# Optimization experiments

Measured on AMD Instinct MI355X. Metric: run time of the kernel, lower is better.

## Reference

```python
import jax, jax.numpy as jnp
import numpy as np

D = 500  # hidden width hard-coded in the module

def _lrelu(x):
    # nn.LeakyReLU default negative_slope = 0.01
    return jnp.where(x > 0, x, 0.01 * x)

def setup_inputs() -> dict:
    key = jax.random.key(0)
    ks = jax.random.split(key, 20)
    T, B = 2048, 64
    inp = {
        "pitches": jax.random.normal(ks[0], (T, B, 128), dtype=jnp.float32),
        "velocities": jax.random.normal(ks[1], (T, B, 128), dtype=jnp.float32),
        "durations": jax.random.uniform(ks[2], (T, B, 1), dtype=jnp.float32),
        "steps": jax.random.uniform(ks[3], (T, B, 1), dtype=jnp.float32),
        # learned params (torch Linear convention: W is [out, in])
        "Wp": jax.random.normal(ks[4], (D, 128), dtype=jnp.float32) * 0.05,
        "bp": jax.random.normal(ks[5], (D,), dtype=jnp.float32) * 0.05,
        "Wv": jax.random.normal(ks[6], (D, 128), dtype=jnp.float32) * 0.05,
        "bv": jax.random.normal(ks[7], (D,), dtype=jnp.float32) * 0.05,
        "Wd": jax.random.normal(ks[8], (D, 1), dtype=jnp.float32) * 0.05,
        "bd": jax.random.normal(ks[9], (D,), dtype=jnp.float32) * 0.05,
        "Ws": jax.random.normal(ks[10], (D, 1), dtype=jnp.float32) * 0.05,
        "bs": jax.random.normal(ks[11], (D,), dtype=jnp.float32) * 0.05,
        "W1": jax.random.normal(ks[12], (D, D), dtype=jnp.float32) * 0.05,
        "b1": jax.random.normal(ks[13], (D,), dtype=jnp.float32) * 0.05,
        "W2": jax.random.normal(ks[14], (D, D), dtype=jnp.float32) * 0.05,
        "b2": jax.random.normal(ks[15], (D,), dtype=jnp.float32) * 0.05,
        "Wi": jax.random.normal(ks[16], (D, D), dtype=jnp.float32) * 0.05,
        "bi": jax.random.normal(ks[17], (D,), dtype=jnp.float32) * 0.05,
        "W3": jax.random.normal(ks[18], (1, D), dtype=jnp.float32) * 0.05,
        "b3": jax.random.normal(ks[19], (1,), dtype=jnp.float32) * 0.05,
    }
    return inp

def reference(pitches, velocities, durations, steps,
              Wp, bp, Wv, bv, Wd, bd, Ws, bs,
              W1, b1, W2, b2, Wi, bi, W3, b3):
    # Note: in the original torch code the LSTMCell output is computed then
    # discarded (overwritten), and `info` at step t depends only on inputs at
    # step t. Thus the final output depends only on the last timestep through
    # the embed-sum -> LeakyReLU MLP -> linear_intermediate chain.
    # Vectorized over all T timesteps (same per-step math as the loop body).
    add = (jnp.einsum('tbi,oi->tbo', pitches, Wp) + bp
           + jnp.einsum('tbi,oi->tbo', velocities, Wv) + bv
           + jnp.einsum('tbi,oi->tbo', durations, Wd) + bd
           + jnp.einsum('tbi,oi->tbo', steps, Ws) + bs)      # [T,B,500]
    h = _lrelu(jnp.einsum('tbi,oi->tbo', add, W1) + b1)
    h = _lrelu(jnp.einsum('tbi,oi->tbo', h, W2) + b2)
    info = jnp.einsum('tbi,oi->tbo', h, Wi) + bi              # [T,B,500]
    out = jax.nn.sigmoid(info[-1] @ W3.T + b3)                # [B,1]
    return out
```

## Files before the change

kernel.cpp:

```cpp
#include <hip/hip_runtime.h>

#define DD 500
#define BB 64
#define TT 2048
#define KP 128
#define VCHUNKS 32
#define VPSTRIDE 512

__global__ __launch_bounds__(256) void k_embed(
    const float* __restrict__ pitches, const float* __restrict__ velocities,
    const float* __restrict__ durations, const float* __restrict__ steps,
    const float* __restrict__ Wp, const float* __restrict__ bp,
    const float* __restrict__ Wv, const float* __restrict__ bv,
    const float* __restrict__ Wd, const float* __restrict__ bd,
    const float* __restrict__ Wst, const float* __restrict__ bs,
    float* __restrict__ addT)
{
    const int tid = threadIdx.x;
    const int bid = blockIdx.x;

    __shared__ float lds[KP * BB];
    const int b = tid & 63;
    const int o = __builtin_amdgcn_readfirstlane(bid * 4 + (tid >> 6));
    const float* __restrict__ wp = Wp + o * KP;
    const float* __restrict__ wv = Wv + o * KP;

    float a0 = 0.f, a1 = 0.f, a2 = 0.f, a3 = 0.f;

    const float4* Psrc = (const float4*)(pitches + (size_t)(TT - 1) * BB * KP);
    const float4* Vsrc = (const float4*)(velocities + (size_t)(TT - 1) * BB * KP);

    for (int j = tid; j < BB * KP / 4; j += 256) {
        float4 p = Psrc[j];
        int pb = j >> 5;
        int k0 = (j & 31) * 4;
        lds[(k0 + 0) * BB + ((pb + k0 + 0) & 63)] = p.x;
        lds[(k0 + 1) * BB + ((pb + k0 + 1) & 63)] = p.y;
        lds[(k0 + 2) * BB + ((pb + k0 + 2) & 63)] = p.z;
        lds[(k0 + 3) * BB + ((pb + k0 + 3) & 63)] = p.w;
    }
    __syncthreads();
    for (int k = 0; k < KP; k += 4) {
        a0 += lds[(k + 0) * BB + ((b + k + 0) & 63)] * wp[k + 0];
        a1 += lds[(k + 1) * BB + ((b + k + 1) & 63)] * wp[k + 1];
        a2 += lds[(k + 2) * BB + ((b + k + 2) & 63)] * wp[k + 2];
        a3 += lds[(k + 3) * BB + ((b + k + 3) & 63)] * wp[k + 3];
    }
    __syncthreads();

    for (int j = tid; j < BB * KP / 4; j += 256) {
        float4 p = Vsrc[j];
        int pb = j >> 5;
        int k0 = (j & 31) * 4;
        lds[(k0 + 0) * BB + ((pb + k0 + 0) & 63)] = p.x;
        lds[(k0 + 1) * BB + ((pb + k0 + 1) & 63)] = p.y;
        lds[(k0 + 2) * BB + ((pb + k0 + 2) & 63)] = p.z;
        lds[(k0 + 3) * BB + ((pb + k0 + 3) & 63)] = p.w;
    }
    __syncthreads();
    for (int k = 0; k < KP; k += 4) {
        a0 += lds[(k + 0) * BB + ((b + k + 0) & 63)] * wv[k + 0];
        a1 += lds[(k + 1) * BB + ((b + k + 1) & 63)] * wv[k + 1];
        a2 += lds[(k + 2) * BB + ((b + k + 2) & 63)] * wv[k + 2];
        a3 += lds[(k + 3) * BB + ((b + k + 3) & 63)] * wv[k + 3];
    }

    const float dur = durations[(size_t)(TT - 1) * BB + b];
    const float st  = steps[(size_t)(TT - 1) * BB + b];
    addT[o * BB + b] = bp[o] + bv[o] + bd[o] + bs[o]
                     + dur * Wd[o] + st * Wst[o]
                     + (a0 + a1) + (a2 + a3);
}

__global__ __launch_bounds__(256) void k_dense(
    const float* __restrict__ Ain, const float* __restrict__ W,
    const float* __restrict__ bias, float* __restrict__ Aout, int leaky,
    const float* __restrict__ Wi, const float* __restrict__ W3,
    float* __restrict__ vpart)
{
    const int tid = threadIdx.x;
    const int bid = blockIdx.x;

    if (bid >= DD) {
        const int oc = bid - DD;
        const int obeg = oc * 16;
        const int k0 = tid;
        const int k1 = tid + 256;
        float acc0 = 0.f, acc1 = 0.f;
        #pragma unroll
        for (int i = 0; i < 16; ++i) {
            const int o = obeg + i;
            const int oc_ = o < DD ? o : DD - 1;
            const float ww = o < DD ? W3[oc_] : 0.f;
            acc0 += ww * Wi[(size_t)oc_ * DD + k0];
            if (k1 < DD) acc1 += ww * Wi[(size_t)oc_ * DD + k1];
        }
        vpart[oc * VPSTRIDE + k0] = acc0;
        if (k1 < DD) vpart[oc * VPSTRIDE + k1] = acc1;
        return;
    }

    __shared__ float partial[4][BB];
    const int b = tid & 63;
    const int w = tid >> 6;
    const int o = bid;
    const float* __restrict__ wrow = W + o * DD;
    const int kbeg = w * 125;

    float a0 = 0.f, a1 = 0.f, a2 = 0.f, a3 = 0.f;
    float a4 = 0.f, a5 = 0.f, a6 = 0.f, a7 = 0.f;
    #pragma unroll 3
    for (int k = kbeg; k < kbeg + 120; k += 8) {
        a0 += Ain[(k + 0) * BB + b] * wrow[k + 0];
        a1 += Ain[(k + 1) * BB + b] * wrow[k + 1];
        a2 += Ain[(k + 2) * BB + b] * wrow[k + 2];
        a3 += Ain[(k + 3) * BB + b] * wrow[k + 3];
        a4 += Ain[(k + 4) * BB + b] * wrow[k + 4];
        a5 += Ain[(k + 5) * BB + b] * wrow[k + 5];
        a6 += Ain[(k + 6) * BB + b] * wrow[k + 6];
        a7 += Ain[(k + 7) * BB + b] * wrow[k + 7];
    }
    {
        const int k = kbeg + 120;
        a0 += Ain[(k + 0) * BB + b] * wrow[k + 0];
        a1 += Ain[(k + 1) * BB + b] * wrow[k + 1];
        a2 += Ain[(k + 2) * BB + b] * wrow[k + 2];
        a3 += Ain[(k + 3) * BB + b] * wrow[k + 3];
        a4 += Ain[(k + 4) * BB + b] * wrow[k + 4];
    }
    partial[w][b] = ((a0 + a1) + (a2 + a3)) + ((a4 + a5) + (a6 + a7));
    __syncthreads();
    if (w == 0) {
        float acc = bias[o] + (partial[0][b] + partial[1][b])
                            + (partial[2][b] + partial[3][b]);
        if (leaky) acc = acc > 0.f ? acc : 0.01f * acc;
        Aout[o * BB + b] = acc;
    }
}

__global__ __launch_bounds__(1024) void k_out(
    const float* __restrict__ h2T, const float* __restrict__ vpart,
    const float* __restrict__ W3, const float* __restrict__ bi,
    const float* __restrict__ b3, float* __restrict__ out)
{
    __shared__ float vv[DD];
    __shared__ float partial[16][BB];
    const int tid = threadIdx.x;

    if (tid < DD) {
        const int k = tid;
        float s0 = 0.f, s1 = 0.f, s2 = 0.f, s3 = 0.f;
        float s4 = 0.f, s5 = 0.f, s6 = 0.f, s7 = 0.f;
        #pragma unroll
        for (int oc = 0; oc < VCHUNKS; oc += 8) {
            s0 += vpart[(oc + 0) * VPSTRIDE + k];
            s1 += vpart[(oc + 1) * VPSTRIDE + k];
            s2 += vpart[(oc + 2) * VPSTRIDE + k];
            s3 += vpart[(oc + 3) * VPSTRIDE + k];
            s4 += vpart[(oc + 4) * VPSTRIDE + k];
            s5 += vpart[(oc + 5) * VPSTRIDE + k];
            s6 += vpart[(oc + 6) * VPSTRIDE + k];
            s7 += vpart[(oc + 7) * VPSTRIDE + k];
        }
        vv[k] = ((s0 + s1) + (s2 + s3)) + ((s4 + s5) + (s6 + s7));
    }
    __syncthreads();

    const int b = tid & 63;
    const int w = tid >> 6;
    const int kbeg = w * 32;
    const int kend = kbeg + 32 < DD ? kbeg + 32 : DD;

    float accA = 0.f, accB = 0.f, accC = 0.f, accD = 0.f;
    for (int k = kbeg; k < kend; k += 4) {
        accA += h2T[(k + 0) * BB + b] * vv[k + 0];
        accB += h2T[(k + 1) * BB + b] * vv[k + 1];
        accC += h2T[(k + 2) * BB + b] * vv[k + 2];
        accD += h2T[(k + 3) * BB + b] * vv[k + 3];
        accA += W3[k + 0] * bi[k + 0];
        accB += W3[k + 1] * bi[k + 1];
        accC += W3[k + 2] * bi[k + 2];
        accD += W3[k + 3] * bi[k + 3];
    }
    partial[w][b] = (accA + accB) + (accC + accD);
    __syncthreads();
    if (w == 0) {
        float s = b3[0];
        #pragma unroll
        for (int i = 0; i < 16; ++i) s += partial[i][b];
        out[b] = 1.f / (1.f + __expf(-s));
    }
}

extern "C" void kernel_launch(void* const* d_in, const int* in_sizes, int n_in,
                              void* d_out, int out_size, void* d_ws, size_t ws_size,
                              hipStream_t stream)
{
    const float* pitches    = (const float*)d_in[0];
    const float* velocities = (const float*)d_in[1];
    const float* durations  = (const float*)d_in[2];
    const float* steps      = (const float*)d_in[3];
    const float* Wp  = (const float*)d_in[4];
    const float* bp  = (const float*)d_in[5];
    const float* Wv  = (const float*)d_in[6];
    const float* bv  = (const float*)d_in[7];
    const float* Wd  = (const float*)d_in[8];
    const float* bd  = (const float*)d_in[9];
    const float* Wst = (const float*)d_in[10];
    const float* bs  = (const float*)d_in[11];
    const float* W1  = (const float*)d_in[12];
    const float* b1  = (const float*)d_in[13];
    const float* W2  = (const float*)d_in[14];
    const float* b2  = (const float*)d_in[15];
    const float* Wi  = (const float*)d_in[16];
    const float* bi  = (const float*)d_in[17];
    const float* W3  = (const float*)d_in[18];
    const float* b3  = (const float*)d_in[19];

    float* ws    = (float*)d_ws;
    float* addT  = ws;
    float* h1T   = ws + 32000;
    float* h2T   = ws + 64000;
    float* vpart = ws + 96000;

    float* out = (float*)d_out;

    k_embed<<<125, 256, 0, stream>>>(pitches, velocities, durations, steps,
                                     Wp, bp, Wv, bv, Wd, bd, Wst, bs, addT);
    k_dense<<<DD + VCHUNKS, 256, 0, stream>>>(addT, W1, b1, h1T, 1,
                                              Wi, W3, vpart);
    k_dense<<<DD, 256, 0, stream>>>(h1T, W2, b2, h2T, 1, Wi, W3, vpart);
    k_out<<<1, 1024, 0, stream>>>(h2T, vpart, W3, bi, b3, out);
}
```

Measured before the change: 186.8 us.

## Fuse output reduction into second dense layer with atomics and last-block ticket

Moves the Wi·W3 collapse and the constant term into the embedding kernel, and folds the final dot-product and sigmoid into the second dense layer. Each block atomically adds its contribution into 16 slot accumulators, and the last block to arrive (tracked by a ticket counter) sums them and writes the output. This removes one kernel launch and the serial single-block tail reduction. In exchange it adds atomic traffic and a grid-wide last-block pattern, and float atomics make the summation order nondeterministic.

```diff
diff --git a/kernel.cpp b/kernel.cpp
--- a/kernel.cpp
+++ b/kernel.cpp
@@ -6,83 +6,39 @@
 #define KP 128
 #define VCHUNKS 32
 #define VPSTRIDE 512
-
-__global__ __launch_bounds__(256) void k_embed(
+#define NSLOTS 16
+
+
+__global__ __launch_bounds__(256) void k_front(
     const float* __restrict__ pitches, const float* __restrict__ velocities,
     const float* __restrict__ durations, const float* __restrict__ steps,
     const float* __restrict__ Wp, const float* __restrict__ bp,
     const float* __restrict__ Wv, const float* __restrict__ bv,
     const float* __restrict__ Wd, const float* __restrict__ bd,
     const float* __restrict__ Wst, const float* __restrict__ bs,
-    float* __restrict__ addT)
+    const float* __restrict__ Wi, const float* __restrict__ W3,
+    const float* __restrict__ bi, const float* __restrict__ b3,
+    float* __restrict__ addT, float* __restrict__ vpart,
+    float* __restrict__ outacc, float* __restrict__ ticket,
+    float* __restrict__ cval)
 {
     const int tid = threadIdx.x;
     const int bid = blockIdx.x;
 
-    __shared__ float lds[KP * BB];
-    const int b = tid & 63;
-    const int o = __builtin_amdgcn_readfirstlane(bid * 4 + (tid >> 6));
-    const float* __restrict__ wp = Wp + o * KP;
-    const float* __restrict__ wv = Wv + o * KP;
-
-    float a0 = 0.f, a1 = 0.f, a2 = 0.f, a3 = 0.f;
-
-    const float4* Psrc = (const float4*)(pitches + (size_t)(TT - 1) * BB * KP);
-    const float4* Vsrc = (const float4*)(velocities + (size_t)(TT - 1) * BB * KP);
-
-    for (int j = tid; j < BB * KP / 4; j += 256) {
-        float4 p = Psrc[j];
-        int pb = j >> 5;
-        int k0 = (j & 31) * 4;
-        lds[(k0 + 0) * BB + ((pb + k0 + 0) & 63)] = p.x;
-        lds[(k0 + 1) * BB + ((pb + k0 + 1) & 63)] = p.y;
-        lds[(k0 + 2) * BB + ((pb + k0 + 2) & 63)] = p.z;
-        lds[(k0 + 3) * BB + ((pb + k0 + 3) & 63)] = p.w;
-    }
-    __syncthreads();
-    for (int k = 0; k < KP; k += 4) {
-        a0 += lds[(k + 0) * BB + ((b + k + 0) & 63)] * wp[k + 0];
-        a1 += lds[(k + 1) * BB + ((b + k + 1) & 63)] * wp[k + 1];
-        a2 += lds[(k + 2) * BB + ((b + k + 2) & 63)] * wp[k + 2];
-        a3 += lds[(k + 3) * BB + ((b + k + 3) & 63)] * wp[k + 3];
-    }
-    __syncthreads();
-
-    for (int j = tid; j < BB * KP / 4; j += 256) {
-        float4 p = Vsrc[j];
-        int pb = j >> 5;
-        int k0 = (j & 31) * 4;
-        lds[(k0 + 0) * BB + ((pb + k0 + 0) & 63)] = p.x;
-        lds[(k0 + 1) * BB + ((pb + k0 + 1) & 63)] = p.y;
-        lds[(k0 + 2) * BB + ((pb + k0 + 2) & 63)] = p.z;
-        lds[(k0 + 3) * BB + ((pb + k0 + 3) & 63)] = p.w;
-    }
-    __syncthreads();
-    for (int k = 0; k < KP; k += 4) {
-        a0 += lds[(k + 0) * BB + ((b + k + 0) & 63)] * wv[k + 0];
-        a1 += lds[(k + 1) * BB + ((b + k + 1) & 63)] * wv[k + 1];
-        a2 += lds[(k + 2) * BB + ((b + k + 2) & 63)] * wv[k + 2];
-        a3 += lds[(k + 3) * BB + ((b + k + 3) & 63)] * wv[k + 3];
-    }
-
-    const float dur = durations[(size_t)(TT - 1) * BB + b];
-    const float st  = steps[(size_t)(TT - 1) * BB + b];
-    addT[o * BB + b] = bp[o] + bv[o] + bd[o] + bs[o]
-                     + dur * Wd[o] + st * Wst[o]
-                     + (a0 + a1) + (a2 + a3);
-}
-
-__global__ __launch_bounds__(256) void k_dense(
-    const float* __restrict__ Ain, const float* __restrict__ W,
-    const float* __restrict__ bias, float* __restrict__ Aout, int leaky,
-    const float* __restrict__ Wi, const float* __restrict__ W3,
-    float* __restrict__ vpart)
-{
-    const int tid = threadIdx.x;
-    const int bid = blockIdx.x;
-
-    if (bid >= DD) {
-        const int oc = bid - DD;
+    if (bid >= 125) {
+        const int oc = bid - 125;
+        if (oc == 0) {
+            ((float4*)outacc)[tid] = make_float4(0.f, 0.f, 0.f, 0.f);
+            if (tid == 0) *(unsigned int*)ticket = 0u;
+            if (tid < 64) {
+                float cs = 0.f;
+                for (int j = tid; j < DD; j += 64) cs += W3[j] * bi[j];
+                #pragma unroll
+                for (int off = 32; off > 0; off >>= 1)
+                    cs += __shfl_xor(cs, off);
+                if (tid == 0) cval[0] = cs + b3[0];
+            }
+        }
         const int obeg = oc * 16;
         const int k0 = tid;
         const int k1 = tid + 256;
@@ -100,10 +56,68 @@
         return;
     }
 
+    __shared__ float lds[KP * BB];
+    const int b = tid & 63;
+    const int o = __builtin_amdgcn_readfirstlane(bid * 4 + (tid >> 6));
+    const float* __restrict__ wp = Wp + o * KP;
+    const float* __restrict__ wv = Wv + o * KP;
+
+    float a0 = 0.f, a1 = 0.f, a2 = 0.f, a3 = 0.f;
+
+    const float4* Psrc = (const float4*)(pitches + (size_t)(TT - 1) * BB * KP);
+    const float4* Vsrc = (const float4*)(velocities + (size_t)(TT - 1) * BB * KP);
+
+    for (int j = tid; j < BB * KP / 4; j += 256) {
+        float4 p = Psrc[j];
+        int pb = j >> 5;
+        int k0 = (j & 31) * 4;
+        lds[(k0 + 0) * BB + ((pb + k0 + 0) & 63)] = p.x;
+        lds[(k0 + 1) * BB + ((pb + k0 + 1) & 63)] = p.y;
+        lds[(k0 + 2) * BB + ((pb + k0 + 2) & 63)] = p.z;
+        lds[(k0 + 3) * BB + ((pb + k0 + 3) & 63)] = p.w;
+    }
+    __syncthreads();
+    for (int k = 0; k < KP; k += 4) {
+        a0 += lds[(k + 0) * BB + ((b + k + 0) & 63)] * wp[k + 0];
+        a1 += lds[(k + 1) * BB + ((b + k + 1) & 63)] * wp[k + 1];
+        a2 += lds[(k + 2) * BB + ((b + k + 2) & 63)] * wp[k + 2];
+        a3 += lds[(k + 3) * BB + ((b + k + 3) & 63)] * wp[k + 3];
+    }
+    __syncthreads();
+
+    for (int j = tid; j < BB * KP / 4; j += 256) {
+        float4 p = Vsrc[j];
+        int pb = j >> 5;
+        int k0 = (j & 31) * 4;
+        lds[(k0 + 0) * BB + ((pb + k0 + 0) & 63)] = p.x;
+        lds[(k0 + 1) * BB + ((pb + k0 + 1) & 63)] = p.y;
+        lds[(k0 + 2) * BB + ((pb + k0 + 2) & 63)] = p.z;
+        lds[(k0 + 3) * BB + ((pb + k0 + 3) & 63)] = p.w;
+    }
+    __syncthreads();
+    for (int k = 0; k < KP; k += 4) {
+        a0 += lds[(k + 0) * BB + ((b + k + 0) & 63)] * wv[k + 0];
+        a1 += lds[(k + 1) * BB + ((b + k + 1) & 63)] * wv[k + 1];
+        a2 += lds[(k + 2) * BB + ((b + k + 2) & 63)] * wv[k + 2];
+        a3 += lds[(k + 3) * BB + ((b + k + 3) & 63)] * wv[k + 3];
+    }
+
+    const float dur = durations[(size_t)(TT - 1) * BB + b];
+    const float st  = steps[(size_t)(TT - 1) * BB + b];
+    addT[o * BB + b] = bp[o] + bv[o] + bd[o] + bs[o]
+                     + dur * Wd[o] + st * Wst[o]
+                     + (a0 + a1) + (a2 + a3);
+}
+
+__global__ __launch_bounds__(256) void k_dense1(
+    const float* __restrict__ Ain, const float* __restrict__ W,
+    const float* __restrict__ bias, float* __restrict__ Aout)
+{
     __shared__ float partial[4][BB];
+    const int tid = threadIdx.x;
     const int b = tid & 63;
     const int w = tid >> 6;
-    const int o = bid;
+    const int o = blockIdx.x;
     const float* __restrict__ wrow = W + o * DD;
     const int kbeg = w * 125;
 
@@ -133,62 +147,77 @@
     if (w == 0) {
         float acc = bias[o] + (partial[0][b] + partial[1][b])
                             + (partial[2][b] + partial[3][b]);
-        if (leaky) acc = acc > 0.f ? acc : 0.01f * acc;
+        acc = acc > 0.f ? acc : 0.01f * acc;
         Aout[o * BB + b] = acc;
     }
 }
 
-__global__ __launch_bounds__(1024) void k_out(
-    const float* __restrict__ h2T, const float* __restrict__ vpart,
-    const float* __restrict__ W3, const float* __restrict__ bi,
-    const float* __restrict__ b3, float* __restrict__ out)
-{
-    __shared__ float vv[DD];
-    __shared__ float partial[16][BB];
+__global__ __launch_bounds__(256) void k_dense2_out(
+    const float* __restrict__ Ain, const float* __restrict__ W,
+    const float* __restrict__ bias, const float* __restrict__ vpart,
+    const float* __restrict__ cval, float* __restrict__ outacc,
+    float* __restrict__ ticket, float* __restrict__ out)
+{
+    __shared__ float partial[4][BB];
+    __shared__ float vvs;
     const int tid = threadIdx.x;
-
-    if (tid < DD) {
-        const int k = tid;
-        float s0 = 0.f, s1 = 0.f, s2 = 0.f, s3 = 0.f;
-        float s4 = 0.f, s5 = 0.f, s6 = 0.f, s7 = 0.f;
-        #pragma unroll
-        for (int oc = 0; oc < VCHUNKS; oc += 8) {
-            s0 += vpart[(oc + 0) * VPSTRIDE + k];
-            s1 += vpart[(oc + 1) * VPSTRIDE + k];
-            s2 += vpart[(oc + 2) * VPSTRIDE + k];
-            s3 += vpart[(oc + 3) * VPSTRIDE + k];
-            s4 += vpart[(oc + 4) * VPSTRIDE + k];
-            s5 += vpart[(oc + 5) * VPSTRIDE + k];
-            s6 += vpart[(oc + 6) * VPSTRIDE + k];
-            s7 += vpart[(oc + 7) * VPSTRIDE + k];
-        }
-        vv[k] = ((s0 + s1) + (s2 + s3)) + ((s4 + s5) + (s6 + s7));
-    }
-    __syncthreads();
-
     const int b = tid & 63;
     const int w = tid >> 6;
-    const int kbeg = w * 32;
-    const int kend = kbeg + 32 < DD ? kbeg + 32 : DD;
-
-    float accA = 0.f, accB = 0.f, accC = 0.f, accD = 0.f;
-    for (int k = kbeg; k < kend; k += 4) {
-        accA += h2T[(k + 0) * BB + b] * vv[k + 0];
-        accB += h2T[(k + 1) * BB + b] * vv[k + 1];
-        accC += h2T[(k + 2) * BB + b] * vv[k + 2];
-        accD += h2T[(k + 3) * BB + b] * vv[k + 3];
-        accA += W3[k + 0] * bi[k + 0];
-        accB += W3[k + 1] * bi[k + 1];
-        accC += W3[k + 2] * bi[k + 2];
-        accD += W3[k + 3] * bi[k + 3];
-    }
-    partial[w][b] = (accA + accB) + (accC + accD);
-    __syncthreads();
+    const int o = blockIdx.x;
+    const float* __restrict__ wrow = W + o * DD;
+    const int kbeg = w * 125;
+
+    float vvl = 0.f;
+    if (w == 1 && b < 32) vvl = vpart[b * VPSTRIDE + o];
+
+    float a0 = 0.f, a1 = 0.f, a2 = 0.f, a3 = 0.f;
+    float a4 = 0.f, a5 = 0.f, a6 = 0.f, a7 = 0.f;
+    #pragma unroll 3
+    for (int k = kbeg; k < kbeg + 120; k += 8) {
+        a0 += Ain[(k + 0) * BB + b] * wrow[k + 0];
+        a1 += Ain[(k + 1) * BB + b] * wrow[k + 1];
+        a2 += Ain[(k + 2) * BB + b] * wrow[k + 2];
+        a3 += Ain[(k + 3) * BB + b] * wrow[k + 3];
+        a4 += Ain[(k + 4) * BB + b] * wrow[k + 4];
+        a5 += Ain[(k + 5) * BB + b] * wrow[k + 5];
+        a6 += Ain[(k + 6) * BB + b] * wrow[k + 6];
+        a7 += Ain[(k + 7) * BB + b] * wrow[k + 7];
+    }
+    {
+        const int k = kbeg + 120;
+        a0 += Ain[(k + 0) * BB + b] * wrow[k + 0];
+        a1 += Ain[(k + 1) * BB + b] * wrow[k + 1];
+        a2 += Ain[(k + 2) * BB + b] * wrow[k + 2];
+        a3 += Ain[(k + 3) * BB + b] * wrow[k + 3];
+        a4 += Ain[(k + 4) * BB + b] * wrow[k + 4];
+    }
+    partial[w][b] = ((a0 + a1) + (a2 + a3)) + ((a4 + a5) + (a6 + a7));
+
+    if (w == 1) {
+        #pragma unroll
+        for (int off = 16; off > 0; off >>= 1) vvl += __shfl_xor(vvl, off);
+        if (b == 0) vvs = vvl;
+    }
+    __syncthreads();
+
     if (w == 0) {
-        float s = b3[0];
-        #pragma unroll
-        for (int i = 0; i < 16; ++i) s += partial[i][b];
-        out[b] = 1.f / (1.f + __expf(-s));
+        float acc = bias[o] + (partial[0][b] + partial[1][b])
+                            + (partial[2][b] + partial[3][b]);
+        acc = acc > 0.f ? acc : 0.01f * acc;
+        const float contrib = vvs * acc;
+        atomicAdd(&outacc[(o & (NSLOTS - 1)) * BB + b], contrib);
+        __threadfence();
+        int old = 0;
+        if (b == 0) old = (int)atomicAdd((unsigned int*)ticket, 1u);
+        old = __shfl(old, 0);
+        if (old == DD - 1) {
+            __threadfence();
+            float s = cval[0];
+            #pragma unroll
+            for (int slot = 0; slot < NSLOTS; ++slot)
+                s += atomicAdd(&outacc[slot * BB + b], 0.0f);
+            out[b] = 1.f / (1.f + __expf(-s));
+        }
     }
 }
 
@@ -217,18 +246,21 @@
     const float* W3  = (const float*)d_in[18];
     const float* b3  = (const float*)d_in[19];
 
-    float* ws    = (float*)d_ws;
-    float* addT  = ws;
-    float* h1T   = ws + 32000;
-    float* h2T   = ws + 64000;
-    float* vpart = ws + 96000;
+    float* ws     = (float*)d_ws;
+    float* addT   = ws;
+    float* h1T    = ws + 32000;
+    float* vpart  = ws + 64000;
+    float* outacc = ws + 80384;
+    float* ticket = ws + 81408;
+    float* cval   = ws + 81409;
 
     float* out = (float*)d_out;
 
-    k_embed<<<125, 256, 0, stream>>>(pitches, velocities, durations, steps,
-                                     Wp, bp, Wv, bv, Wd, bd, Wst, bs, addT);
-    k_dense<<<DD + VCHUNKS, 256, 0, stream>>>(addT, W1, b1, h1T, 1,
-                                              Wi, W3, vpart);
-    k_dense<<<DD, 256, 0, stream>>>(h1T, W2, b2, h2T, 1, Wi, W3, vpart);
-    k_out<<<1, 1024, 0, stream>>>(h2T, vpart, W3, bi, b3, out);
-}
+    k_front<<<157, 256, 0, stream>>>(pitches, velocities, durations, steps,
+                                     Wp, bp, Wv, bv, Wd, bd, Wst, bs,
+                                     Wi, W3, bi, b3,
+                                     addT, vpart, outacc, ticket, cval);
+    k_dense1<<<DD, 256, 0, stream>>>(addT, W1, b1, h1T);
+    k_dense2_out<<<DD, 256, 0, stream>>>(h1T, W2, b2, vpart, cval,
+                                         outacc, ticket, out);
+}
```

Result: no change. 188.3 us (+0.8%).
